# Optimization experiments

Measured on AMD Instinct MI355X. Metric: run time of the kernel, lower is better.

The kernel has to match this reference:

```python
import jax, jax.numpy as jnp
import numpy as np
from functools import partial


def deform_sample(inp, dy, dx):
    """Bilinear sample inp[b,c] at (y+dy[b,c,y,x], x+dx[b,c,y,x]) with zero padding.
    inp, dy, dx: [B, C, H, W] -> [B, C, H, W]. Matches torchvision deform_conv2d
    with 1x1 kernel and offset_groups == C (one offset pair per channel)."""
    B, C, H, W = inp.shape
    ys = jnp.arange(H, dtype=inp.dtype)[None, None, :, None] + dy  # [B,C,H,W]
    xs = jnp.arange(W, dtype=inp.dtype)[None, None, None, :] + dx
    y0f = jnp.floor(ys)
    x0f = jnp.floor(xs)
    wy = ys - y0f
    wx = xs - x0f
    y0 = y0f.astype(jnp.int32)
    x0 = x0f.astype(jnp.int32)
    flat = inp.reshape(B, C, H * W)

    def gather(yi, xi):
        valid = (yi >= 0) & (yi < H) & (xi >= 0) & (xi < W)
        idx = jnp.clip(yi, 0, H - 1) * W + jnp.clip(xi, 0, W - 1)
        v = jnp.take_along_axis(flat, idx.reshape(B, C, H * W), axis=2).reshape(B, C, H, W)
        return jnp.where(valid, v, jnp.zeros((), inp.dtype))

    return ((1 - wy) * (1 - wx) * gather(y0, x0)
            + (1 - wy) * wx * gather(y0, x0 + 1)
            + wy * (1 - wx) * gather(y0 + 1, x0)
            + wy * wx * gather(y0 + 1, x0 + 1))


def atm_layer(x, offset, w_weight, w_bias, h_weight, h_bias, local_weight, local_bias,
              fc1_w, fc1_b, fc2_w, fc2_b, proj_w, proj_b):
    B, H, W, C = x.shape
    x_nchw = jnp.transpose(x, (0, 3, 1, 2))  # [B,C,H,W]
    zeros = jnp.zeros_like(x_nchw)

    # ATM along w: offset[:, :C] is x-offset (offset_t[:,1::2]), y-offset 0
    sw = deform_sample(x_nchw, zeros, offset[:, :C])
    w = jnp.einsum('bchw,oc->bhwo', sw, w_weight) + w_bias  # [B,H,W,C]

    # ATM along h: offset[:, C:] is y-offset (offset_t[:,0::2]), x-offset 0
    sh = deform_sample(x_nchw, offset[:, C:], zeros)
    h = jnp.einsum('bchw,oc->bhwo', sh, h_weight) + h_bias

    # depthwise 5x5 conv, padding 2
    c = jax.lax.conv_general_dilated(
        x_nchw, local_weight, window_strides=(1, 1), padding=((2, 2), (2, 2)),
        feature_group_count=C, dimension_numbers=('NCHW', 'OIHW', 'NCHW'))
    c = jnp.transpose(c, (0, 2, 3, 1)) + local_bias  # [B,H,W,C]

    # gating MLP: global average -> fc1 -> GELU -> fc2 -> softmax over 3 branches
    a = (w + h + c).mean(axis=(1, 2))  # [B,C]
    a = jax.nn.gelu(a @ fc1_w.T + fc1_b, approximate=False)
    a = a @ fc2_w.T + fc2_b  # [B,3C]
    a = jnp.transpose(a.reshape(B, C, 3), (2, 0, 1))  # [3,B,C]
    a = jax.nn.softmax(a, axis=0)[:, :, None, None, :]  # [3,B,1,1,C]

    out = w * a[0] + h * a[1] + c * a[2]
    out = out @ proj_w.T + proj_b
    return out


def setup_inputs() -> dict:
    C = 256
    B, H, W = 16, 64, 64
    key = jax.random.key(0)
    ks = jax.random.split(key, 16)
    bnd = 1.0 / np.sqrt(C)
    hid = C // 4
    return {
        'x': jax.random.normal(ks[0], (B, H, W, C), jnp.float32),
        'offset': jax.random.normal(ks[1], (B, 2 * C, H, W), jnp.float32),
        'w_weight': jax.random.uniform(ks[2], (C, C), jnp.float32, -bnd, bnd),
        'w_bias': jax.random.uniform(ks[3], (C,), jnp.float32, -bnd, bnd),
        'h_weight': jax.random.uniform(ks[4], (C, C), jnp.float32, -bnd, bnd),
        'h_bias': jax.random.uniform(ks[5], (C,), jnp.float32, -bnd, bnd),
        'local_weight': jax.random.uniform(ks[6], (C, 1, 5, 5), jnp.float32, -0.2, 0.2),
        'local_bias': jax.random.uniform(ks[7], (C,), jnp.float32, -0.2, 0.2),
        'fc1_w': jax.random.uniform(ks[8], (hid, C), jnp.float32, -bnd, bnd),
        'fc1_b': jax.random.uniform(ks[9], (hid,), jnp.float32, -bnd, bnd),
        'fc2_w': jax.random.uniform(ks[10], (3 * C, hid), jnp.float32, -1.0 / np.sqrt(hid), 1.0 / np.sqrt(hid)),
        'fc2_b': jax.random.uniform(ks[11], (3 * C,), jnp.float32, -1.0 / np.sqrt(hid), 1.0 / np.sqrt(hid)),
        'proj_w': jax.random.uniform(ks[12], (C, C), jnp.float32, -bnd, bnd),
        'proj_b': jax.random.uniform(ks[13], (C,), jnp.float32, -bnd, bnd),
    }


def reference(x, offset, w_weight, w_bias, h_weight, h_bias, local_weight, local_bias,
              fc1_w, fc1_b, fc2_w, fc2_b, proj_w, proj_b):
    return atm_layer(x, offset, w_weight, w_bias, h_weight, h_bias, local_weight,
                     local_bias, fc1_w, fc1_b, fc2_w, fc2_b, proj_w, proj_b)
```

## Files before the change

kernel.cpp:

```cpp
#include <hip/hip_runtime.h>
#include <hip/hip_bf16.h>

typedef _Float16 half4_t __attribute__((ext_vector_type(4)));
typedef _Float16 half8 __attribute__((ext_vector_type(8)));
typedef float f32x4 __attribute__((ext_vector_type(4)));

#define BB 16
#define HH 64
#define WW2 64
#define CC 256

__global__ __launch_bounds__(256) void k_trans(const float* __restrict__ off,
                                               _Float16* __restrict__ offAT,
                                               _Float16* __restrict__ offBT)
{
  __shared__ _Float16 tile[64][65];
  const int blk = blockIdx.x;
  const int st   = blk & 63;
  const int cht  = (blk >> 6) & 3;
  const int half = (blk >> 8) & 1;
  const int b    = blk >> 9;
  const int t = threadIdx.x;

  const int s0 = st * 64;
  const int ch0 = half * 256 + cht * 64;
  const float* src = off + ((size_t)b * 512 + ch0) * 4096 + s0;
  const int sl = t & 63;
  #pragma unroll
  for (int p = 0; p < 16; p++) {
    int chl = (t >> 6) + p * 4;
    tile[chl][sl] = (_Float16)src[(size_t)chl * 4096 + sl];
  }
  __syncthreads();

  _Float16* dst = (half == 0) ? offAT : offBT;
  #pragma unroll
  for (int p = 0; p < 2; p++) {
    int pl = (t >> 3) + p * 32;
    int c8 = (t & 7) * 8;
    half8 hv;
    #pragma unroll
    for (int r = 0; r < 8; r++) hv[r] = tile[c8 + r][pl];
    int s = s0 + pl;
    size_t pix = (half == 0) ? ((size_t)b * 4096 + s)
                             : ((size_t)b * 4096 + (s & 63) * 64 + (s >> 6));
    *(half8*)(dst + pix * 256 + cht * 64 + c8) = hv;
  }
}

__global__ __launch_bounds__(256) void k_row(
    const float* __restrict__ x, const _Float16* offA,
    const float* __restrict__ lw,
    _Float16* swb, _Float16* __restrict__ cvb,
    float* __restrict__ ssw, float* __restrict__ scv)
{
  __shared__ _Float16 xr[WW2 * CC];

  const int work = (blockIdx.x & 7) * 128 + (blockIdx.x >> 3);
  const int b = work >> 6, y = work & 63;
  const int t = threadIdx.x;
  const int c = t;

  const float* xrow_src = x + (size_t)(b * HH + y) * WW2 * CC;
  #pragma unroll
  for (int p = 0; p < 16; p++) {
    int i = p * 1024 + t * 4;
    float4 v = *(const float4*)(xrow_src + i);
    half4_t h = {(_Float16)v.x, (_Float16)v.y, (_Float16)v.z, (_Float16)v.w};
    *(half4_t*)(xr + i) = h;
  }

  float wgt[25];
  #pragma unroll
  for (int q = 0; q < 25; q++) wgt[q] = lw[c * 25 + q];
  const float* xb = x + (size_t)b * HH * WW2 * CC + c;
  const float* rp[5];
  bool yv[5];
  #pragma unroll
  for (int ky = 0; ky < 5; ky++) {
    int yy = y + ky - 2;
    yv[ky] = (yy >= 0 && yy < HH);
    rp[ky] = xb + (size_t)(yv[ky] ? yy : 0) * WW2 * CC;
  }
  __syncthreads();

  const _Float16* off_g = offA + ((size_t)b * 4096 + y * 64) * CC + c;
  size_t orow = (size_t)(b * HH + y) * WW2 * CC + c;

  float acc5[5] = {0.f, 0.f, 0.f, 0.f, 0.f};
  float asw = 0.f, acv = 0.f;
  float dx_next = (float)off_g[0];

  #pragma unroll 5
  for (int u = 0; u < 70; ++u) {
    acc5[(u + 2) % 5] = 0.f;
    if (u < 64) {
      float c0 = yv[0] ? rp[0][u * CC] : 0.f;
      float c1 = yv[1] ? rp[1][u * CC] : 0.f;
      float c2 = yv[2] ? rp[2][u * CC] : 0.f;
      float c3 = yv[3] ? rp[3][u * CC] : 0.f;
      float c4 = yv[4] ? rp[4][u * CC] : 0.f;
      #pragma unroll
      for (int kx = 0; kx < 5; kx++) {
        acc5[(u + 7 - kx) % 5] += wgt[0 + kx] * c0 + wgt[5 + kx] * c1 +
                                  wgt[10 + kx] * c2 + wgt[15 + kx] * c3 +
                                  wgt[20 + kx] * c4;
      }
    }
    int xi = u - 2;
    if (xi >= 0 && xi < 64) {
      float dx = dx_next;
      if (xi + 1 < 64) dx_next = (float)off_g[(size_t)(xi + 1) * CC];
      float cv = acc5[(u + 3) % 5];

      float xs = (float)xi + dx;
      float xf = floorf(xs);
      float wx = xs - xf;
      int xq = (int)xf;
      float v0 = (xq >= 0 && xq < WW2) ? (float)xr[xq * CC + c] : 0.f;
      float v1 = (xq + 1 >= 0 && xq + 1 < WW2) ? (float)xr[(xq + 1) * CC + c] : 0.f;
      float swv = (1.f - wx) * v0 + wx * v1;

      size_t oi = orow + (size_t)xi * CC;
      swb[oi] = (_Float16)swv;
      cvb[oi] = (_Float16)cv;
      asw += swv; acv += cv;
    }
  }

  atomicAdd(&ssw[b * CC + c], asw);
  atomicAdd(&scv[b * CC + c], acv);
}

__global__ __launch_bounds__(256) void k_col(
    const float* __restrict__ x, const _Float16* __restrict__ offBT,
    _Float16* __restrict__ shb, float* __restrict__ ssh)
{
  __shared__ _Float16 xc[HH * CC];
  const int work = (blockIdx.x & 7) * 128 + (blockIdx.x >> 3);
  const int b = work >> 6, xi = work & 63;
  const int t = threadIdx.x;
  const int c = t;

  #pragma unroll
  for (int p = 0; p < 16; p++) {
    int yy = p * 4 + (t >> 6);
    int c4 = (t & 63) * 4;
    float4 v = *(const float4*)(x + ((size_t)(b * HH + yy) * WW2 + xi) * CC + c4);
    half4_t h = {(_Float16)v.x, (_Float16)v.y, (_Float16)v.z, (_Float16)v.w};
    *(half4_t*)(xc + yy * CC + c4) = h;
  }
  __syncthreads();

  const _Float16* obt = offBT + ((size_t)(b * WW2 + xi) * HH) * CC + c;
  float ash = 0.f;
  for (int yy = 0; yy < HH; yy++) {
    float dy = (float)obt[yy * CC];
    float ys = (float)yy + dy;
    float yf = floorf(ys);
    float wy = ys - yf;
    int yq = (int)yf;
    float u0 = (yq >= 0 && yq < HH) ? (float)xc[yq * CC + c] : 0.f;
    float u1 = (yq + 1 >= 0 && yq + 1 < HH) ? (float)xc[(yq + 1) * CC + c] : 0.f;
    float shv = (1.f - wy) * u0 + wy * u1;
    shb[((size_t)(b * HH + yy) * WW2 + xi) * CC + c] = (_Float16)shv;
    ash += shv;
  }
  atomicAdd(&ssh[b * CC + c], ash);
}

__global__ __launch_bounds__(256) void k_gate(
    const float* __restrict__ ssw, const float* __restrict__ ssh, const float* __restrict__ scv,
    const float* __restrict__ Ww, const float* __restrict__ bw,
    const float* __restrict__ Wh, const float* __restrict__ bh,
    const float* __restrict__ blc,
    const float* __restrict__ fc1w, const float* __restrict__ fc1b,
    const float* __restrict__ fc2w, const float* __restrict__ fc2b,
    float* __restrict__ gate)
{
  __shared__ float sswl[CC], sshl[CC], avgl[CC], tl[64];
  const int b = blockIdx.x, tid = threadIdx.x;
  sswl[tid] = ssw[b * CC + tid];
  sshl[tid] = ssh[b * CC + tid];
  __syncthreads();

  float acc = scv[b * CC + tid];
  for (int c = 0; c < CC; c++)
    acc += sswl[c] * Ww[tid * CC + c] + sshl[c] * Wh[tid * CC + c];
  avgl[tid] = acc * (1.f / (HH * WW2)) + bw[tid] + bh[tid] + blc[tid];
  __syncthreads();

  if (tid < 64) {
    float a = fc1b[tid];
    for (int o = 0; o < CC; o++) a += avgl[o] * fc1w[tid * CC + o];
    tl[tid] = 0.5f * a * (1.f + erff(a * 0.70710678118654752f));
  }
  __syncthreads();

  float g[3];
  #pragma unroll
  for (int j = 0; j < 3; j++) {
    float a = fc2b[tid * 3 + j];
    for (int k = 0; k < 64; k++) a += tl[k] * fc2w[(tid * 3 + j) * 64 + k];
    g[j] = a;
  }
  float m = fmaxf(g[0], fmaxf(g[1], g[2]));
  float e0 = expf(g[0] - m), e1 = expf(g[1] - m), e2 = expf(g[2] - m);
  float inv = 1.f / (e0 + e1 + e2);
  gate[(0 * BB + b) * CC + tid] = e0 * inv;
  gate[(1 * BB + b) * CC + tid] = e1 * inv;
  gate[(2 * BB + b) * CC + tid] = e2 * inv;
}

__global__ __launch_bounds__(256) void k_prep(
    const float* __restrict__ gate,
    const float* __restrict__ Ww, const float* __restrict__ Wh,
    const float* __restrict__ bw, const float* __restrict__ bh,
    const float* __restrict__ blc,
    _Float16* __restrict__ Bp, float* __restrict__ bcomb)
{
  const int id = blockIdx.x;
  const int b = id >> 8, n = id & 255;
  const int k = threadIdx.x;
  float a0 = gate[(0 * BB + b) * CC + n];
  float a1 = gate[(1 * BB + b) * CC + n];
  float a2 = gate[(2 * BB + b) * CC + n];
  size_t base = (size_t)id * 512;
  Bp[base + k]       = (_Float16)(a0 * Ww[n * CC + k]);
  Bp[base + 256 + k] = (_Float16)(a1 * Wh[n * CC + k]);
  if (k == 0) bcomb[id] = a0 * bw[n] + a1 * bh[n] + a2 * blc[n];
}

__global__ __launch_bounds__(256) void k_cvt(const float* __restrict__ pw,
                                             _Float16* __restrict__ pf)
{
  int i = blockIdx.x * 256 + threadIdx.x;
  pf[i] = (_Float16)pw[i];
}

#define CPAD 260
__global__ __launch_bounds__(256) void k_fused(
    const _Float16* __restrict__ swb, const _Float16* __restrict__ shb,
    const _Float16* __restrict__ Bp, const float* __restrict__ bcomb,
    const float* __restrict__ a2g, const _Float16* __restrict__ cvb,
    const _Float16* __restrict__ pf, const float* __restrict__ pb,
    float* __restrict__ out)
{
  __shared__ _Float16 comb[64 * CPAD];

  const int work = (blockIdx.x & 7) * 128 + (blockIdx.x >> 3);
  const int r0 = work * 64;
  const int b = work >> 6;
  const int tid = threadIdx.x;
  const int wid = tid >> 6, l = tid & 63;
  const int n0 = wid * 64;
  const int lr = l & 15;
  const int kg = (l >> 4) * 8;
  const int jr = (l >> 4) * 4;

  const _Float16* ap0 = swb + (size_t)(r0 + lr) * CC + kg;
  const _Float16* ap1 = shb + (size_t)(r0 + lr) * CC + kg;
  const _Float16* bp  = Bp + ((size_t)b * CC + n0 + lr) * 512 + kg;

  f32x4 acc[4][4];
  #pragma unroll
  for (int mi = 0; mi < 4; mi++)
    #pragma unroll
    for (int ni = 0; ni < 4; ni++) acc[mi][ni] = (f32x4){0.f, 0.f, 0.f, 0.f};

  #pragma unroll
  for (int ks = 0; ks < 16; ks++) {
    half8 a[4], bbv[4];
    #pragma unroll
    for (int mi = 0; mi < 4; mi++) {
      const _Float16* s = (ks < 8) ? (ap0 + (size_t)mi * 16 * CC + ks * 32)
                                   : (ap1 + (size_t)mi * 16 * CC + (ks - 8) * 32);
      a[mi] = *(const half8*)s;
    }
    #pragma unroll
    for (int ni = 0; ni < 4; ni++)
      bbv[ni] = *(const half8*)(bp + (size_t)ni * 16 * 512 + ks * 32);
    #pragma unroll
    for (int mi = 0; mi < 4; mi++)
      #pragma unroll
      for (int ni = 0; ni < 4; ni++)
        acc[mi][ni] = __builtin_amdgcn_mfma_f32_16x16x32_f16(a[mi], bbv[ni], acc[mi][ni], 0, 0, 0);
  }

  #pragma unroll
  for (int ni = 0; ni < 4; ni++) {
    int col = n0 + ni * 16 + lr;
    float bc = bcomb[b * CC + col];
    float a2 = a2g[b * CC + col];
    #pragma unroll
    for (int mi = 0; mi < 4; mi++) {
      #pragma unroll
      for (int j = 0; j < 4; j++) {
        int r = mi * 16 + jr + j;
        size_t idx = (size_t)(r0 + r) * CC + col;
        float v = acc[mi][ni][j] + bc + a2 * (float)cvb[idx];
        comb[r * CPAD + col] = (_Float16)v;
      }
    }
  }
  __syncthreads();

  const _Float16* bp2 = pf + (size_t)(n0 + lr) * CC + kg;

  f32x4 acc2[4][4];
  #pragma unroll
  for (int mi = 0; mi < 4; mi++)
    #pragma unroll
    for (int ni = 0; ni < 4; ni++) acc2[mi][ni] = (f32x4){0.f, 0.f, 0.f, 0.f};

  #pragma unroll
  for (int ks = 0; ks < 8; ks++) {
    half8 a[4], bbv[4];
    #pragma unroll
    for (int mi = 0; mi < 4; mi++) {
      const _Float16* s = comb + (mi * 16 + lr) * CPAD + kg + ks * 32;
      half4_t lo = *(const half4_t*)(s);
      half4_t hi = *(const half4_t*)(s + 4);
      a[mi][0] = lo[0]; a[mi][1] = lo[1]; a[mi][2] = lo[2]; a[mi][3] = lo[3];
      a[mi][4] = hi[0]; a[mi][5] = hi[1]; a[mi][6] = hi[2]; a[mi][7] = hi[3];
    }
    #pragma unroll
    for (int ni = 0; ni < 4; ni++)
      bbv[ni] = *(const half8*)(bp2 + (size_t)ni * 16 * CC + ks * 32);
    #pragma unroll
    for (int mi = 0; mi < 4; mi++)
      #pragma unroll
      for (int ni = 0; ni < 4; ni++)
        acc2[mi][ni] = __builtin_amdgcn_mfma_f32_16x16x32_f16(a[mi], bbv[ni], acc2[mi][ni], 0, 0, 0);
  }

  #pragma unroll
  for (int ni = 0; ni < 4; ni++) {
    int col = n0 + ni * 16 + lr;
    float bias = pb[col];
    #pragma unroll
    for (int mi = 0; mi < 4; mi++) {
      #pragma unroll
      for (int j = 0; j < 4; j++) {
        size_t idx = (size_t)(r0 + mi * 16 + jr + j) * CC + col;
        out[idx] = acc2[mi][ni][j] + bias;
      }
    }
  }
}

extern "C" void kernel_launch(void* const* d_in, const int* in_sizes, int n_in,
                              void* d_out, int out_size, void* d_ws, size_t ws_size,
                              hipStream_t stream)
{
  const float* x    = (const float*)d_in[0];
  const float* off  = (const float*)d_in[1];
  const float* Ww   = (const float*)d_in[2];
  const float* bw   = (const float*)d_in[3];
  const float* Wh   = (const float*)d_in[4];
  const float* bh   = (const float*)d_in[5];
  const float* lw   = (const float*)d_in[6];
  const float* blc  = (const float*)d_in[7];
  const float* fc1w = (const float*)d_in[8];
  const float* fc1b = (const float*)d_in[9];
  const float* fc2w = (const float*)d_in[10];
  const float* fc2b = (const float*)d_in[11];
  const float* pw   = (const float*)d_in[12];
  const float* pb   = (const float*)d_in[13];
  float* out = (float*)d_out;

  char* ws = (char*)d_ws;
  _Float16* shb   = (_Float16*)(ws + 0);
  _Float16* offAT = (_Float16*)(ws + 33554432);
  _Float16* swb   = (_Float16*)(ws + 33554432);
  _Float16* offBT = (_Float16*)(ws + 67108864);
  _Float16* cvb   = (_Float16*)(ws + 67108864);
  _Float16* Bp    = (_Float16*)(ws + 100663296);
  _Float16* pf    = (_Float16*)(ws + 104857600);
  float* sums     = (float*)(ws + 104988672);
  float* gate     = (float*)(ws + 105037824);
  float* bcomb    = (float*)(ws + 105086976);
  float* ssw = sums, *ssh = sums + 4096, *scv = sums + 8192;

  hipMemsetAsync(sums, 0, 3 * 4096 * sizeof(float), stream);
  k_trans<<<8192, 256, 0, stream>>>(off, offAT, offBT);
  k_col<<<BB * WW2, 256, 0, stream>>>(x, offBT, shb, ssh);
  k_row<<<BB * HH, 256, 0, stream>>>(x, offAT, lw, swb, cvb, ssw, scv);
  k_gate<<<BB, 256, 0, stream>>>(ssw, ssh, scv, Ww, bw, Wh, bh, blc,
                                 fc1w, fc1b, fc2w, fc2b, gate);
  k_prep<<<BB * CC, 256, 0, stream>>>(gate, Ww, Wh, bw, bh, blc, Bp, bcomb);
  k_cvt<<<CC, 256, 0, stream>>>(pw, pf);
  k_fused<<<1024, 256, 0, stream>>>(swb, shb, Bp, bcomb, gate + 2 * BB * CC,
                                    cvb, pf, pb, out);
}
```

Measured before the change: 303.3 us.

## Split row deform sampling and depthwise conv into separate kernels

The fused row kernel, which did the width-direction deformable sampling and the 5x5 depthwise conv together, is split in two. k_rows stages an x row in LDS and does the sampling. k_conv has no LDS and computes the conv straight from global memory. Workspace buffers are reassigned so each output overwrites offset data that has already been consumed. The split aims to remove the LDS-limited occupancy and register pressure of the combined kernel, at the cost of an extra launch and a second pass over x.

```diff
diff --git a/kernel.cpp b/kernel.cpp
--- a/kernel.cpp
+++ b/kernel.cpp
@@ -48,11 +48,9 @@
   }
 }
 
-__global__ __launch_bounds__(256) void k_row(
-    const float* __restrict__ x, const _Float16* offA,
-    const float* __restrict__ lw,
-    _Float16* swb, _Float16* __restrict__ cvb,
-    float* __restrict__ ssw, float* __restrict__ scv)
+__global__ __launch_bounds__(256) void k_rows(
+    const float* __restrict__ x, const _Float16* __restrict__ offA,
+    _Float16* __restrict__ swb, float* __restrict__ ssw)
 {
   __shared__ _Float16 xr[WW2 * CC];
 
@@ -69,10 +67,40 @@
     half4_t h = {(_Float16)v.x, (_Float16)v.y, (_Float16)v.z, (_Float16)v.w};
     *(half4_t*)(xr + i) = h;
   }
+  __syncthreads();
+
+  const _Float16* op = offA + ((size_t)b * 4096 + y * 64) * CC + c;
+  _Float16* sp = swb + ((size_t)b * 4096 + y * 64) * CC + c;
+  float asw = 0.f;
+
+  #pragma unroll 8
+  for (int xi = 0; xi < 64; xi++) {
+    float dx = (float)op[(size_t)xi * CC];
+    float xs = (float)xi + dx;
+    float xf = floorf(xs);
+    float wx = xs - xf;
+    int xq = (int)xf;
+    float v0 = (xq >= 0 && xq < WW2) ? (float)xr[xq * CC + c] : 0.f;
+    float v1 = (xq + 1 >= 0 && xq + 1 < WW2) ? (float)xr[(xq + 1) * CC + c] : 0.f;
+    float swv = (1.f - wx) * v0 + wx * v1;
+    sp[(size_t)xi * CC] = (_Float16)swv;
+    asw += swv;
+  }
+  atomicAdd(&ssw[b * CC + c], asw);
+}
+
+__global__ __launch_bounds__(256) void k_conv(
+    const float* __restrict__ x, const float* __restrict__ lw,
+    _Float16* __restrict__ cvb, float* __restrict__ scv)
+{
+  const int work = (blockIdx.x & 7) * 128 + (blockIdx.x >> 3);
+  const int b = work >> 6, y = work & 63;
+  const int c = threadIdx.x;
 
   float wgt[25];
   #pragma unroll
   for (int q = 0; q < 25; q++) wgt[q] = lw[c * 25 + q];
+
   const float* xb = x + (size_t)b * HH * WW2 * CC + c;
   const float* rp[5];
   bool yv[5];
@@ -82,14 +110,10 @@
     yv[ky] = (yy >= 0 && yy < HH);
     rp[ky] = xb + (size_t)(yv[ky] ? yy : 0) * WW2 * CC;
   }
-  __syncthreads();
-
-  const _Float16* off_g = offA + ((size_t)b * 4096 + y * 64) * CC + c;
-  size_t orow = (size_t)(b * HH + y) * WW2 * CC + c;
-
+
+  _Float16* cp = cvb + ((size_t)b * 4096 + y * 64) * CC + c;
   float acc5[5] = {0.f, 0.f, 0.f, 0.f, 0.f};
-  float asw = 0.f, acv = 0.f;
-  float dx_next = (float)off_g[0];
+  float acv = 0.f;
 
   #pragma unroll 5
   for (int u = 0; u < 70; ++u) {
@@ -109,26 +133,11 @@
     }
     int xi = u - 2;
     if (xi >= 0 && xi < 64) {
-      float dx = dx_next;
-      if (xi + 1 < 64) dx_next = (float)off_g[(size_t)(xi + 1) * CC];
       float cv = acc5[(u + 3) % 5];
-
-      float xs = (float)xi + dx;
-      float xf = floorf(xs);
-      float wx = xs - xf;
-      int xq = (int)xf;
-      float v0 = (xq >= 0 && xq < WW2) ? (float)xr[xq * CC + c] : 0.f;
-      float v1 = (xq + 1 >= 0 && xq + 1 < WW2) ? (float)xr[(xq + 1) * CC + c] : 0.f;
-      float swv = (1.f - wx) * v0 + wx * v1;
-
-      size_t oi = orow + (size_t)xi * CC;
-      swb[oi] = (_Float16)swv;
-      cvb[oi] = (_Float16)cv;
-      asw += swv; acv += cv;
-    }
-  }
-
-  atomicAdd(&ssw[b * CC + c], asw);
+      cp[(size_t)xi * CC] = (_Float16)cv;
+      acv += cv;
+    }
+  }
   atomicAdd(&scv[b * CC + c], acv);
 }
 
@@ -153,9 +162,11 @@
   __syncthreads();
 
   const _Float16* obt = offBT + ((size_t)(b * WW2 + xi) * HH) * CC + c;
+  _Float16* hp = shb + ((size_t)(b * HH) * WW2 + xi) * CC + c;
   float ash = 0.f;
-  for (int yy = 0; yy < HH; yy++) {
-    float dy = (float)obt[yy * CC];
+  #pragma unroll 8
+  for (int yy = 0; yy < 64; yy++) {
+    float dy = (float)obt[(size_t)yy * CC];
     float ys = (float)yy + dy;
     float yf = floorf(ys);
     float wy = ys - yf;
@@ -163,7 +174,7 @@
     float u0 = (yq >= 0 && yq < HH) ? (float)xc[yq * CC + c] : 0.f;
     float u1 = (yq + 1 >= 0 && yq + 1 < HH) ? (float)xc[(yq + 1) * CC + c] : 0.f;
     float shv = (1.f - wy) * u0 + wy * u1;
-    shb[((size_t)(b * HH + yy) * WW2 + xi) * CC + c] = (_Float16)shv;
+    hp[(size_t)yy * WW2 * CC] = (_Float16)shv;
     ash += shv;
   }
   atomicAdd(&ssh[b * CC + c], ash);
@@ -372,9 +383,9 @@
   char* ws = (char*)d_ws;
   _Float16* shb   = (_Float16*)(ws + 0);
   _Float16* offAT = (_Float16*)(ws + 33554432);
-  _Float16* swb   = (_Float16*)(ws + 33554432);
+  _Float16* cvb   = (_Float16*)(ws + 33554432);
   _Float16* offBT = (_Float16*)(ws + 67108864);
-  _Float16* cvb   = (_Float16*)(ws + 67108864);
+  _Float16* swb   = (_Float16*)(ws + 67108864);
   _Float16* Bp    = (_Float16*)(ws + 100663296);
   _Float16* pf    = (_Float16*)(ws + 104857600);
   float* sums     = (float*)(ws + 104988672);
@@ -385,7 +396,8 @@
   hipMemsetAsync(sums, 0, 3 * 4096 * sizeof(float), stream);
   k_trans<<<8192, 256, 0, stream>>>(off, offAT, offBT);
   k_col<<<BB * WW2, 256, 0, stream>>>(x, offBT, shb, ssh);
-  k_row<<<BB * HH, 256, 0, stream>>>(x, offAT, lw, swb, cvb, ssw, scv);
+  k_rows<<<BB * HH, 256, 0, stream>>>(x, offAT, swb, ssw);
+  k_conv<<<BB * HH, 256, 0, stream>>>(x, lw, cvb, scv);
   k_gate<<<BB, 256, 0, stream>>>(ssw, ssh, scv, Ww, bw, Wh, bh, blc,
                                  fc1w, fc1b, fc2w, fc2b, gate);
   k_prep<<<BB * CC, 256, 0, stream>>>(gate, Ww, Wh, bw, bh, blc, Bp, bcomb);
```

New measurement: 306.0 us. Within noise of the previous version (+0.9%).
